# Kernel tuning notes

Hardware: AMD Instinct MI355X
Metric: run time of the kernel (lower is better)

The kernel has to match this reference:

```python
import jax, jax.numpy as jnp
import numpy as np

HIDDEN = 4096
Q_HEADS = 32
KV_HEADS = 8
HEAD_DIM = 128
MAX_LEN = 8192
PAST_LEN = 4096
SEQ_LEN = 16
BSZ = 1
REPEAT_KV = Q_HEADS // KV_HEADS
SCALE = HEAD_DIM ** (-0.5)


def _apply_rope(x):
    # x: [b, h, s, d]; positions start at 0 (faithful to source, even for cached k)
    s, d = x.shape[2], x.shape[3]
    half = d // 2
    positions = jnp.arange(s, dtype=x.dtype)
    inv_freq = jnp.arange(half, dtype=x.dtype) / half
    angles = positions[:, None] * inv_freq[None, :]          # [s, half]
    sin = jnp.sin(angles)[None, None]
    cos = jnp.cos(angles)[None, None]
    x_even, x_odd = x[..., :half], x[..., half:]
    return jnp.concatenate([x_even * cos - x_odd * sin,
                            x_even * sin + x_odd * cos], axis=-1)


def setup_inputs() -> dict:
    key = jax.random.key(0)
    ks = jax.random.split(key, 5)
    qkv_dim = (Q_HEADS + 2 * KV_HEADS) * HEAD_DIM
    x = jax.random.normal(ks[0], (BSZ, SEQ_LEN, HIDDEN), dtype=jnp.float32)
    w_qkv = jax.random.normal(ks[1], (qkv_dim, HIDDEN), dtype=jnp.float32) * 0.02
    w_out = jax.random.normal(ks[2], (HIDDEN, Q_HEADS * HEAD_DIM), dtype=jnp.float32) * 0.02
    cache_k = jax.random.normal(ks[3], (1, KV_HEADS, MAX_LEN, HEAD_DIM), dtype=jnp.float32)
    cache_v = jax.random.normal(ks[4], (1, KV_HEADS, MAX_LEN, HEAD_DIM), dtype=jnp.float32)
    return {"x": x, "w_qkv": w_qkv, "w_out": w_out, "cache_k": cache_k, "cache_v": cache_v}


def reference(x, w_qkv, w_out, cache_k, cache_v):
    bsz, seq_len, _ = x.shape
    qkv = jnp.einsum('bsh,oh->bso', x, w_qkv)
    q_size = Q_HEADS * HEAD_DIM
    kv_size = KV_HEADS * HEAD_DIM
    q = qkv[..., :q_size].reshape(bsz, seq_len, Q_HEADS, HEAD_DIM).transpose(0, 2, 1, 3)
    k = qkv[..., q_size:q_size + kv_size].reshape(bsz, seq_len, KV_HEADS, HEAD_DIM).transpose(0, 2, 1, 3)
    v = qkv[..., q_size + kv_size:].reshape(bsz, seq_len, KV_HEADS, HEAD_DIM).transpose(0, 2, 1, 3)
    q = _apply_rope(q)
    k = _apply_rope(k)
    # KV-cache append (static slice positions)
    cache_k = cache_k.at[:, :, PAST_LEN:PAST_LEN + seq_len, :].set(k)
    cache_v = cache_v.at[:, :, PAST_LEN:PAST_LEN + seq_len, :].set(v)
    key_len = PAST_LEN + seq_len
    key = cache_k[:, :, :key_len, :]
    value = cache_v[:, :, :key_len, :]
    if REPEAT_KV > 1:  # GQA broadcast
        key = jnp.repeat(key, REPEAT_KV, axis=1)
        value = jnp.repeat(value, REPEAT_KV, axis=1)
    scores = jnp.einsum('bhqd,bhkd->bhqk', q, key) * SCALE
    q_pos = jnp.arange(seq_len)
    k_pos = jnp.arange(key_len)
    mask = (k_pos[None, :] <= q_pos[:, None] + PAST_LEN).astype(scores.dtype)
    scores = scores + (1.0 - mask)[None, None] * -10000.0
    weights = jax.nn.softmax(scores, axis=-1)
    out = jnp.einsum('bhqk,bhkd->bhqd', weights, value)
    out = out.transpose(0, 2, 1, 3).reshape(bsz, seq_len, Q_HEADS * HEAD_DIM)
    return jnp.einsum('bso,ho->bsh', out, w_out)
```

## Files before the change

kernel.cpp:

```cpp
#include <hip/hip_runtime.h>
#include <hip/hip_bf16.h>

typedef __bf16 bf16;
typedef __bf16 bf16x4 __attribute__((ext_vector_type(4)));
typedef __bf16 bf16x8 __attribute__((ext_vector_type(8)));
typedef float f32x4 __attribute__((ext_vector_type(4)));

#define HID 4096
#define QKVN 6144
#define NQH 32
#define NKVH 8
#define HD 128
#define MAXLEN 8192
#define PAST 4096
#define SQ 16
#define SCALE 0.08838834764831845f
#define NEGBIG (-30000.0f)

#define KS 8
#define KPB 512
#define WSTR 520
#define ACH 64
#define NCH 65

__device__ __forceinline__ f32x4 mfma16(bf16x8 a, bf16x8 b, f32x4 c) {
  return __builtin_amdgcn_mfma_f32_16x16x32_bf16(a, b, c, 0, 0, 0);
}

__device__ __forceinline__ bf16x8 load8f(const float* p) {
  const f32x4* q = (const f32x4*)p;
  f32x4 a = q[0], b = q[1];
  bf16x8 r;
  r[0] = (bf16)a[0]; r[1] = (bf16)a[1]; r[2] = (bf16)a[2]; r[3] = (bf16)a[3];
  r[4] = (bf16)b[0]; r[5] = (bf16)b[1]; r[6] = (bf16)b[2]; r[7] = (bf16)b[3];
  return r;
}

__device__ __forceinline__ int fmidx(int k, int m) {
  return ((k >> 3) * 16 + m) * 8 + (k & 7);
}

__global__ __launch_bounds__(256) void xprep_kernel(const float* __restrict__ x,
                                                    bf16* __restrict__ xf) {
  int id = blockIdx.x * 256 + threadIdx.x;
  int m = id & 15, o = id >> 4;
  bf16x8 v = load8f(x + (size_t)m * HID + o * 8);
  *(bf16x8*)(xf + (size_t)(o * 16 + m) * 8) = v;
}

template <int NT>
__global__ __launch_bounds__(256) void gemm16_kernel(const bf16* __restrict__ afrag,
                                                     const float* __restrict__ w,
                                                     float* __restrict__ partial) {
  int tid = threadIdx.x, lane = tid & 63, wv = tid >> 6;
  int l15 = lane & 15, quad = lane >> 4;
  int nt = blockIdx.x % NT, kq = blockIdx.x / NT;

  __shared__ __align__(16) bf16 Wt[16 * WSTR];
  __shared__ __align__(16) float red[4][64][4];

  const float* wb = w + (size_t)(nt * 16) * HID + kq * KPB;
  int r2 = tid >> 7;
  int c4 = tid & 127;
  f32x4 stg[8];
#pragma unroll
  for (int it = 0; it < 8; ++it)
    stg[it] = *(const f32x4*)(wb + (size_t)(it * 2 + r2) * HID + c4 * 4);

  int obase = kq * 64 + wv * 16;
  bf16x8 af[4];
#pragma unroll
  for (int kk = 0; kk < 4; ++kk)
    af[kk] = *(const bf16x8*)(afrag + (size_t)((obase + kk * 4 + quad) * 16 + l15) * 8);

#pragma unroll
  for (int it = 0; it < 8; ++it) {
    bf16x4 t;
    t[0] = (bf16)stg[it][0]; t[1] = (bf16)stg[it][1];
    t[2] = (bf16)stg[it][2]; t[3] = (bf16)stg[it][3];
    *(bf16x4*)(Wt + (it * 2 + r2) * WSTR + c4 * 4) = t;
  }
  __syncthreads();

  f32x4 acc = {0.f, 0.f, 0.f, 0.f};
#pragma unroll
  for (int kk = 0; kk < 4; ++kk) {
    bf16x8 b = *(const bf16x8*)(Wt + l15 * WSTR + wv * 128 + kk * 32 + quad * 8);
    acc = mfma16(af[kk], b, acc);
  }

  *(f32x4*)(&red[wv][lane][0]) = acc;
  __syncthreads();
  if (wv == 0) {
#pragma unroll
    for (int r = 0; r < 4; ++r) {
      float v = red[0][lane][r] + red[1][lane][r] + red[2][lane][r] + red[3][lane][r];
      partial[((size_t)(kq * NT + nt) * 16 + (quad * 4 + r)) * 16 + l15] = v;
    }
  }
}

__device__ __forceinline__ float sum_part(const float* p, int NT, int n, int m) {
  float s = 0.f;
#pragma unroll
  for (int q = 0; q < KS; ++q)
    s += p[((size_t)(q * NT + (n >> 4)) * 16 + m) * 16 + (n & 15)];
  return s;
}

__global__ __launch_bounds__(256) void qkv_finish_kernel(const float* __restrict__ pq,
                                                         bf16* __restrict__ Qf,
                                                         bf16* __restrict__ Kf,
                                                         bf16* __restrict__ Vn) {
  int id = blockIdx.x * 256 + threadIdx.x;
  if (id < 32768) {
    int qh = id >> 10, m = (id >> 6) & 15, j = id & 63;
    float e = sum_part(pq, 384, qh * 128 + j, m);
    float o = sum_part(pq, 384, qh * 128 + 64 + j, m);
    float sn, co;
    __sincosf((float)m * (float)j * (1.0f / 64.0f), &sn, &co);
    Qf[qh * 2048 + fmidx(j, m)] = (bf16)((e * co - o * sn) * SCALE);
    Qf[qh * 2048 + fmidx(j + 64, m)] = (bf16)((e * sn + o * co) * SCALE);
  } else if (id < 40960) {
    int v = id - 32768;
    int kvh = v >> 10, m = (v >> 6) & 15, j = v & 63;
    float e = sum_part(pq, 384, 4096 + kvh * 128 + j, m);
    float o = sum_part(pq, 384, 4096 + kvh * 128 + 64 + j, m);
    float sn, co;
    __sincosf((float)m * (float)j * (1.0f / 64.0f), &sn, &co);
    Kf[kvh * 2048 + fmidx(j, m)] = (bf16)(e * co - o * sn);
    Kf[kvh * 2048 + fmidx(j + 64, m)] = (bf16)(e * sn + o * co);
  } else if (id < 57344) {
    int v = id - 40960;
    int kvh = v >> 11, m = (v >> 7) & 15, d = v & 127;
    Vn[kvh * 2048 + m * 128 + d] = (bf16)sum_part(pq, 384, 5120 + kvh * 128 + d, m);
  }
}

template <bool NEW>
__device__ void attn_body(int kvh, int c,
                          const float* __restrict__ ck, const float* __restrict__ cv,
                          const bf16* __restrict__ Qf, const bf16* __restrict__ Kf,
                          const bf16* __restrict__ Vn,
                          bf16* __restrict__ Opart, float* __restrict__ ml,
                          bf16* Kt, bf16* Vt, bf16* Pl) {
  int tid = threadIdx.x, lane = tid & 63, wv = tid >> 6;
  int l15 = lane & 15, quad = lane >> 4;
  int qh = kvh * 4 + wv;
  int cs = c * ACH;

  bf16x8 af[4];
#pragma unroll
  for (int kk = 0; kk < 4; ++kk)
    af[kk] = *(const bf16x8*)(Qf + qh * 2048 + ((kk * 4 + quad) * 16 + l15) * 8);

  if (!NEW) {
    {
      int kr = tid >> 5;
      int kc4 = tid & 31;
      f32x4 kst[8];
#pragma unroll
      for (int it = 0; it < 8; ++it)
        kst[it] = *(const f32x4*)(ck + ((size_t)(kvh * MAXLEN + cs + it * 8 + kr)) * HD + kc4 * 4);
      int key = tid & 63, dg = tid >> 6;
      f32x4 vst[8];
#pragma unroll
      for (int q4 = 0; q4 < 8; ++q4)
        vst[q4] = *(const f32x4*)(cv + ((size_t)(kvh * MAXLEN + cs + key)) * HD + dg * 32 + q4 * 4);
#pragma unroll
      for (int it = 0; it < 8; ++it) {
        bf16x4 t;
        t[0] = (bf16)kst[it][0]; t[1] = (bf16)kst[it][1];
        t[2] = (bf16)kst[it][2]; t[3] = (bf16)kst[it][3];
        *(bf16x4*)(Kt + (it * 8 + kr) * 136 + kc4 * 4) = t;
      }
#pragma unroll
      for (int q4 = 0; q4 < 8; ++q4)
#pragma unroll
        for (int i = 0; i < 4; ++i)
          Vt[(dg * 32 + q4 * 4 + i) * 72 + key] = (bf16)vst[q4][i];
    }
  } else {
    int key = tid >> 4, dg8 = tid & 15;
    bf16x8 v = *(const bf16x8*)(Vn + kvh * 2048 + key * 128 + dg8 * 8);
#pragma unroll
    for (int i = 0; i < 8; ++i) {
      Vt[(dg8 * 8 + i) * 72 + key] = v[i];
      Vt[(dg8 * 8 + i) * 72 + 16 + key] = (bf16)0.f;
    }
  }
  __syncthreads();

  constexpr int NT = NEW ? 1 : 4;
  f32x4 sc[NT];
  if (!NEW) {
#pragma unroll
    for (int nt = 0; nt < NT; ++nt) {
      f32x4 acc = {0.f, 0.f, 0.f, 0.f};
#pragma unroll
      for (int kk = 0; kk < 4; ++kk) {
        bf16x8 b = *(const bf16x8*)(Kt + (nt * 16 + l15) * 136 + kk * 32 + quad * 8);
        acc = mfma16(af[kk], b, acc);
      }
      sc[nt] = acc;
    }
  } else {
    f32x4 acc = {0.f, 0.f, 0.f, 0.f};
#pragma unroll
    for (int kk = 0; kk < 4; ++kk) {
      bf16x8 b = *(const bf16x8*)(Kf + kvh * 2048 + ((kk * 4 + quad) * 16 + l15) * 8);
      acc = mfma16(af[kk], b, acc);
    }
#pragma unroll
    for (int r = 0; r < 4; ++r)
      if (l15 > quad * 4 + r) acc[r] = NEGBIG;
    sc[0] = acc;
  }

  float mx[4], sm[4];
#pragma unroll
  for (int r = 0; r < 4; ++r) {
    float v = sc[0][r];
#pragma unroll
    for (int nt = 1; nt < NT; ++nt) v = fmaxf(v, sc[nt][r]);
    v = fmaxf(v, __shfl_xor(v, 1));
    v = fmaxf(v, __shfl_xor(v, 2));
    v = fmaxf(v, __shfl_xor(v, 4));
    v = fmaxf(v, __shfl_xor(v, 8));
    mx[r] = v;
  }
#pragma unroll
  for (int nt = 0; nt < NT; ++nt)
#pragma unroll
    for (int r = 0; r < 4; ++r) sc[nt][r] = __expf(sc[nt][r] - mx[r]);
#pragma unroll
  for (int r = 0; r < 4; ++r) {
    float v = 0.f;
#pragma unroll
    for (int nt = 0; nt < NT; ++nt) v += sc[nt][r];
    v += __shfl_xor(v, 1);
    v += __shfl_xor(v, 2);
    v += __shfl_xor(v, 4);
    v += __shfl_xor(v, 8);
    sm[r] = v;
  }

  bf16* Pw = Pl + wv * 16 * 72;
#pragma unroll
  for (int nt = 0; nt < NT; ++nt)
#pragma unroll
    for (int r = 0; r < 4; ++r)
      Pw[(quad * 4 + r) * 72 + nt * 16 + l15] = (bf16)sc[nt][r];
  if (NEW) {
#pragma unroll
    for (int r = 0; r < 4; ++r)
      Pw[(quad * 4 + r) * 72 + 16 + l15] = (bf16)0.f;
  }
  __syncthreads();

  constexpr int KI = NEW ? 1 : 2;
  int rowblk = ((kvh * NCH + c) * 4 + wv) * 16;
  bf16* ob = Opart + (size_t)rowblk * 128;
#pragma unroll
  for (int nt2 = 0; nt2 < 8; ++nt2) {
    f32x4 acc = {0.f, 0.f, 0.f, 0.f};
#pragma unroll
    for (int kk = 0; kk < KI; ++kk) {
      bf16x8 a = *(const bf16x8*)(Pw + l15 * 72 + kk * 32 + quad * 8);
      bf16x8 b = *(const bf16x8*)(Vt + (nt2 * 16 + l15) * 72 + kk * 32 + quad * 8);
      acc = mfma16(a, b, acc);
    }
#pragma unroll
    for (int r = 0; r < 4; ++r)
      ob[(quad * 4 + r) * 128 + nt2 * 16 + l15] = (bf16)acc[r];
  }
  if (l15 == 0) {
#pragma unroll
    for (int r = 0; r < 4; ++r) {
      ml[(size_t)(rowblk + quad * 4 + r) * 2] = mx[r];
      ml[(size_t)(rowblk + quad * 4 + r) * 2 + 1] = sm[r];
    }
  }
}

__global__ __launch_bounds__(256) void attn_kernel(const float* __restrict__ ck,
                                                   const float* __restrict__ cv,
                                                   const bf16* __restrict__ Qf,
                                                   const bf16* __restrict__ Kf,
                                                   const bf16* __restrict__ Vn,
                                                   bf16* __restrict__ Opart,
                                                   float* __restrict__ ml) {
  __shared__ __align__(16) bf16 KtL[64 * 136];
  __shared__ __align__(16) bf16 VtL[128 * 72];
  __shared__ __align__(16) bf16 PL[4 * 16 * 72];
  int c = blockIdx.x % NCH;
  int kvh = blockIdx.x / NCH;
  if (c == NCH - 1)
    attn_body<true>(kvh, c, ck, cv, Qf, Kf, Vn, Opart, ml, KtL, VtL, PL);
  else
    attn_body<false>(kvh, c, ck, cv, Qf, Kf, Vn, Opart, ml, KtL, VtL, PL);
}

__global__ __launch_bounds__(256) void combine_kernel(const bf16* __restrict__ Opart,
                                                      const float* __restrict__ ml,
                                                      bf16* __restrict__ attfm) {
  int tid = threadIdx.x, lane = tid & 63, wv = tid >> 6;
  int qh = blockIdx.x >> 4, srow = blockIdx.x & 15;
  int kvh = qh >> 2, lw = qh & 3;
  size_t rowblk0 = ((size_t)(kvh * NCH) * 4 + lw) * 16 + srow;

  float mw = NEGBIG;
#pragma unroll 4
  for (int c = wv; c < NCH; c += 4)
    mw = fmaxf(mw, ml[(rowblk0 + (size_t)c * 64) * 2]);

  float a0 = 0.f, a1 = 0.f, Lw = 0.f;
#pragma unroll 2
  for (int c = wv; c < NCH; c += 4) {
    const float* mlc = ml + (rowblk0 + (size_t)c * 64) * 2;
    float wc = __expf(mlc[0] - mw);
    Lw += wc * mlc[1];
    const bf16* oc = Opart + (rowblk0 + (size_t)c * 64) * 128;
    a0 += wc * (float)oc[lane];
    a1 += wc * (float)oc[64 + lane];
  }

  __shared__ float sm_m[4], sm_l[4];
  __shared__ float sm_a[4][128];
  if (lane == 0) { sm_m[wv] = mw; sm_l[wv] = Lw; }
  sm_a[wv][lane] = a0;
  sm_a[wv][64 + lane] = a1;
  __syncthreads();

  if (wv == 0) {
    float M = fmaxf(fmaxf(sm_m[0], sm_m[1]), fmaxf(sm_m[2], sm_m[3]));
    float s0 = __expf(sm_m[0] - M), s1 = __expf(sm_m[1] - M);
    float s2 = __expf(sm_m[2] - M), s3 = __expf(sm_m[3] - M);
    float L = s0 * sm_l[0] + s1 * sm_l[1] + s2 * sm_l[2] + s3 * sm_l[3];
    float inv = 1.f / L;
    float A0 = s0 * sm_a[0][lane] + s1 * sm_a[1][lane] + s2 * sm_a[2][lane] + s3 * sm_a[3][lane];
    float A1 = s0 * sm_a[0][64 + lane] + s1 * sm_a[1][64 + lane] +
               s2 * sm_a[2][64 + lane] + s3 * sm_a[3][64 + lane];
    int k1 = qh * 128 + lane, k2 = k1 + 64;
    attfm[fmidx(k1, srow)] = (bf16)(A0 * inv);
    attfm[fmidx(k2, srow)] = (bf16)(A1 * inv);
  }
}

__global__ __launch_bounds__(256) void proj_reduce_kernel(const float* __restrict__ pp,
                                                          float* __restrict__ out) {
  int flat = blockIdx.x * 256 + threadIdx.x;
  int m = flat >> 10, n = (flat & 1023) * 4;
  f32x4 s = {0.f, 0.f, 0.f, 0.f};
#pragma unroll
  for (int q = 0; q < KS; ++q)
    s += *(const f32x4*)(pp + ((size_t)(q * 256 + (n >> 4)) * 16 + m) * 16 + (n & 15));
  *(f32x4*)(out + (size_t)m * HID + n) = s;
}

extern "C" void kernel_launch(void* const* d_in, const int* in_sizes, int n_in,
                              void* d_out, int out_size, void* d_ws, size_t ws_size,
                              hipStream_t stream) {
  const float* x       = (const float*)d_in[0];
  const float* w_qkv   = (const float*)d_in[1];
  const float* w_out   = (const float*)d_in[2];
  const float* cache_k = (const float*)d_in[3];
  const float* cache_v = (const float*)d_in[4];
  float* out = (float*)d_out;

  char* p = (char*)d_ws;
  bf16*  Xfrag = (bf16*)p;               p += (size_t)16 * HID * 2;
  float* partQ = (float*)p;              p += (size_t)KS * 384 * 256 * 4;
  bf16*  Qf    = (bf16*)p;               p += (size_t)NQH * 2048 * 2;
  bf16*  Kf    = (bf16*)p;               p += (size_t)NKVH * 2048 * 2;
  bf16*  Vn    = (bf16*)p;               p += (size_t)NKVH * 2048 * 2;
  bf16*  Opart = (bf16*)p;               p += (size_t)NKVH * NCH * 4 * 16 * 128 * 2;
  float* ml    = (float*)p;              p += (size_t)NKVH * NCH * 4 * 16 * 2 * 4;
  bf16*  attfm = (bf16*)p;               p += (size_t)16 * HID * 2;
  float* partP = (float*)p;              p += (size_t)KS * 256 * 256 * 4;

  hipLaunchKernelGGL(xprep_kernel, dim3(32), dim3(256), 0, stream, x, Xfrag);
  hipLaunchKernelGGL((gemm16_kernel<384>), dim3(384 * KS), dim3(256), 0, stream, Xfrag, w_qkv, partQ);
  hipLaunchKernelGGL(qkv_finish_kernel, dim3(224), dim3(256), 0, stream, partQ, Qf, Kf, Vn);
  hipLaunchKernelGGL(attn_kernel, dim3(NKVH * NCH), dim3(256), 0, stream,
                     cache_k, cache_v, Qf, Kf, Vn, Opart, ml);
  hipLaunchKernelGGL(combine_kernel, dim3(512), dim3(256), 0, stream, Opart, ml, attfm);
  hipLaunchKernelGGL((gemm16_kernel<256>), dim3(256 * KS), dim3(256), 0, stream, attfm, w_out, partP);
  hipLaunchKernelGGL(proj_reduce_kernel, dim3(64), dim3(256), 0, stream, partP, out);
}
```

Baseline: 257.5 us.

## Fuse x conversion into QKV GEMM and use atomic split-K for output projection

Drops the separate xprep kernel: the QKV GEMM now reads fp32 x directly and converts it to bf16 fragments inline. It also drops the proj_reduce kernel. The output GEMM accumulates its split-K partials into the output with atomicAdd, and the combine kernel zeroes the output beforehand. This removes two launches and the partP round trip through memory. The cost is uncoalesced strided loads of x and float atomics, which make the summation order nondeterministic.

```diff
diff --git a/kernel.cpp b/kernel.cpp
--- a/kernel.cpp
+++ b/kernel.cpp
@@ -40,18 +40,10 @@
   return ((k >> 3) * 16 + m) * 8 + (k & 7);
 }
 
-__global__ __launch_bounds__(256) void xprep_kernel(const float* __restrict__ x,
-                                                    bf16* __restrict__ xf) {
-  int id = blockIdx.x * 256 + threadIdx.x;
-  int m = id & 15, o = id >> 4;
-  bf16x8 v = load8f(x + (size_t)m * HID + o * 8);
-  *(bf16x8*)(xf + (size_t)(o * 16 + m) * 8) = v;
-}
-
-template <int NT>
-__global__ __launch_bounds__(256) void gemm16_kernel(const bf16* __restrict__ afrag,
+template <int NT, bool AF32, bool ATOMIC, int OSTR>
+__global__ __launch_bounds__(256) void gemm16_kernel(const void* __restrict__ aptr,
                                                      const float* __restrict__ w,
-                                                     float* __restrict__ partial) {
+                                                     float* __restrict__ outp) {
   int tid = threadIdx.x, lane = tid & 63, wv = tid >> 6;
   int l15 = lane & 15, quad = lane >> 4;
   int nt = blockIdx.x % NT, kq = blockIdx.x / NT;
@@ -67,11 +59,19 @@
   for (int it = 0; it < 8; ++it)
     stg[it] = *(const f32x4*)(wb + (size_t)(it * 2 + r2) * HID + c4 * 4);
 
-  int obase = kq * 64 + wv * 16;
   bf16x8 af[4];
-#pragma unroll
-  for (int kk = 0; kk < 4; ++kk)
-    af[kk] = *(const bf16x8*)(afrag + (size_t)((obase + kk * 4 + quad) * 16 + l15) * 8);
+  if constexpr (AF32) {
+    const float* ab = (const float*)aptr + (size_t)l15 * HID + kq * KPB + wv * 128 + quad * 8;
+#pragma unroll
+    for (int kk = 0; kk < 4; ++kk)
+      af[kk] = load8f(ab + kk * 32);
+  } else {
+    int obase = kq * 64 + wv * 16;
+    const bf16* ab = (const bf16*)aptr;
+#pragma unroll
+    for (int kk = 0; kk < 4; ++kk)
+      af[kk] = *(const bf16x8*)(ab + (size_t)((obase + kk * 4 + quad) * 16 + l15) * 8);
+  }
 
 #pragma unroll
   for (int it = 0; it < 8; ++it) {
@@ -95,7 +95,11 @@
 #pragma unroll
     for (int r = 0; r < 4; ++r) {
       float v = red[0][lane][r] + red[1][lane][r] + red[2][lane][r] + red[3][lane][r];
-      partial[((size_t)(kq * NT + nt) * 16 + (quad * 4 + r)) * 16 + l15] = v;
+      if constexpr (ATOMIC) {
+        atomicAdd(outp + (size_t)(quad * 4 + r) * OSTR + nt * 16 + l15, v);
+      } else {
+        outp[((size_t)(kq * NT + nt) * 16 + (quad * 4 + r)) * 16 + l15] = v;
+      }
     }
   }
 }
@@ -303,11 +307,17 @@
 
 __global__ __launch_bounds__(256) void combine_kernel(const bf16* __restrict__ Opart,
                                                       const float* __restrict__ ml,
-                                                      bf16* __restrict__ attfm) {
+                                                      bf16* __restrict__ attfm,
+                                                      float* __restrict__ out) {
   int tid = threadIdx.x, lane = tid & 63, wv = tid >> 6;
   int qh = blockIdx.x >> 4, srow = blockIdx.x & 15;
   int kvh = qh >> 2, lw = qh & 3;
   size_t rowblk0 = ((size_t)(kvh * NCH) * 4 + lw) * 16 + srow;
+
+  if (tid < 32) {
+    f32x4 z = {0.f, 0.f, 0.f, 0.f};
+    *(f32x4*)(out + (size_t)(blockIdx.x * 32 + tid) * 4) = z;
+  }
 
   float mw = NEGBIG;
 #pragma unroll 4
@@ -347,17 +357,6 @@
   }
 }
 
-__global__ __launch_bounds__(256) void proj_reduce_kernel(const float* __restrict__ pp,
-                                                          float* __restrict__ out) {
-  int flat = blockIdx.x * 256 + threadIdx.x;
-  int m = flat >> 10, n = (flat & 1023) * 4;
-  f32x4 s = {0.f, 0.f, 0.f, 0.f};
-#pragma unroll
-  for (int q = 0; q < KS; ++q)
-    s += *(const f32x4*)(pp + ((size_t)(q * 256 + (n >> 4)) * 16 + m) * 16 + (n & 15));
-  *(f32x4*)(out + (size_t)m * HID + n) = s;
-}
-
 extern "C" void kernel_launch(void* const* d_in, const int* in_sizes, int n_in,
                               void* d_out, int out_size, void* d_ws, size_t ws_size,
                               hipStream_t stream) {
@@ -369,7 +368,6 @@
   float* out = (float*)d_out;
 
   char* p = (char*)d_ws;
-  bf16*  Xfrag = (bf16*)p;               p += (size_t)16 * HID * 2;
   float* partQ = (float*)p;              p += (size_t)KS * 384 * 256 * 4;
   bf16*  Qf    = (bf16*)p;               p += (size_t)NQH * 2048 * 2;
   bf16*  Kf    = (bf16*)p;               p += (size_t)NKVH * 2048 * 2;
@@ -377,14 +375,13 @@
   bf16*  Opart = (bf16*)p;               p += (size_t)NKVH * NCH * 4 * 16 * 128 * 2;
   float* ml    = (float*)p;              p += (size_t)NKVH * NCH * 4 * 16 * 2 * 4;
   bf16*  attfm = (bf16*)p;               p += (size_t)16 * HID * 2;
-  float* partP = (float*)p;              p += (size_t)KS * 256 * 256 * 4;
-
-  hipLaunchKernelGGL(xprep_kernel, dim3(32), dim3(256), 0, stream, x, Xfrag);
-  hipLaunchKernelGGL((gemm16_kernel<384>), dim3(384 * KS), dim3(256), 0, stream, Xfrag, w_qkv, partQ);
+
+  hipLaunchKernelGGL((gemm16_kernel<384, true, false, 0>), dim3(384 * KS), dim3(256), 0, stream,
+                     (const void*)x, w_qkv, partQ);
   hipLaunchKernelGGL(qkv_finish_kernel, dim3(224), dim3(256), 0, stream, partQ, Qf, Kf, Vn);
   hipLaunchKernelGGL(attn_kernel, dim3(NKVH * NCH), dim3(256), 0, stream,
                      cache_k, cache_v, Qf, Kf, Vn, Opart, ml);
-  hipLaunchKernelGGL(combine_kernel, dim3(512), dim3(256), 0, stream, Opart, ml, attfm);
-  hipLaunchKernelGGL((gemm16_kernel<256>), dim3(256 * KS), dim3(256), 0, stream, attfm, w_out, partP);
-  hipLaunchKernelGGL(proj_reduce_kernel, dim3(64), dim3(256), 0, stream, partP, out);
-}
+  hipLaunchKernelGGL(combine_kernel, dim3(512), dim3(256), 0, stream, Opart, ml, attfm, out);
+  hipLaunchKernelGGL((gemm16_kernel<256, false, true, HID>), dim3(256 * KS), dim3(256), 0, stream,
+                     (const void*)attfm, w_out, out);
+}
```

Result: no change. 255.3 us (-0.9%).
